# Kernel optimization log

Measured on AMD Instinct MI355X. Metric: run time of the kernel, lower is better.

The kernel has to match this reference:

```python
import jax, jax.numpy as jnp
import numpy as np
import math

B = 16384
INPUT = 2048
HIDDEN = 2048
PROJ = 1024


def setup_inputs() -> dict:
    key = jax.random.key(0)
    ks = jax.random.split(key, 20)
    stdv = 1.0 / math.sqrt(PROJ)
    u = lambda k, shape: jax.random.uniform(k, shape, jnp.float32, -stdv, stdv)
    return {
        "x_t": jax.random.normal(ks[0], (B, INPUT), jnp.float32),
        "h_t": jax.random.normal(ks[1], (B, PROJ), jnp.float32),
        "c_t": jax.random.normal(ks[2], (B, HIDDEN), jnp.float32),
        "weight_if_x": u(ks[3], (INPUT, 2 * HIDDEN)),
        "weight_if_h": u(ks[4], (PROJ, 2 * HIDDEN)),
        "weight_if_c": u(ks[5], (HIDDEN, 2 * HIDDEN)),
        "bias_i": u(ks[6], (HIDDEN,)),
        "bias_f": u(ks[7], (HIDDEN,)),
        "weight_c_x": u(ks[8], (INPUT, HIDDEN)),
        "weight_c_h": u(ks[9], (PROJ, HIDDEN)),
        "bias_c": u(ks[10], (HIDDEN,)),
        "weight_o_x": u(ks[11], (INPUT, PROJ)),
        "weight_o_h": u(ks[12], (PROJ, PROJ)),
        "weight_o_c": u(ks[13], (HIDDEN, PROJ)),
        "bias_o": u(ks[14], (PROJ,)),
        "weight_r_proj": u(ks[15], (HIDDEN, PROJ)),
        "weight_r_x": u(ks[16], (INPUT, PROJ)),
    }


def reference(x_t, h_t, c_t, weight_if_x, weight_if_h, weight_if_c, bias_i, bias_f,
              weight_c_x, weight_c_h, bias_c, weight_o_x, weight_o_h, weight_o_c,
              bias_o, weight_r_proj, weight_r_x):
    # input/forget gates with peephole on c_t: [B, 2*HIDDEN]
    if_gates = x_t @ weight_if_x + h_t @ weight_if_h + c_t @ weight_if_c
    ingate, forgetgate = jnp.split(if_gates, 2, axis=-1)
    ingate = jax.nn.sigmoid(ingate + bias_i)
    forgetgate = jax.nn.sigmoid(forgetgate + bias_f)
    cellgate = jnp.tanh(x_t @ weight_c_x + h_t @ weight_c_h + bias_c)
    c_new = forgetgate * c_t + ingate * cellgate
    # output gate peeps at new cell state
    outgate = jax.nn.sigmoid(x_t @ weight_o_x + h_t @ weight_o_h + c_new @ weight_o_c + bias_o)
    r_t = jnp.tanh(c_new)
    m_t = r_t @ weight_r_proj
    # input_size != proj_size -> project x for the residual connection
    h_new = outgate * (m_t + x_t @ weight_r_x)
    return (h_new, c_new)
```

## Files before the change

### kernel.cpp

```cpp
#include <hip/hip_runtime.h>
#include <hip/hip_bf16.h>
#include <math.h>

typedef unsigned short u16;
typedef __bf16 bf16x8_t __attribute__((ext_vector_type(8)));
typedef float  f32x4_t  __attribute__((ext_vector_type(4)));
typedef float  f32x8_t  __attribute__((ext_vector_type(8)));
typedef u16    u16x4_t  __attribute__((ext_vector_type(4)));
typedef u16    u16x8_t  __attribute__((ext_vector_type(8)));

__device__ __forceinline__ u16 f2b(float f) {
  unsigned u = __builtin_bit_cast(unsigned, f);
  u += 0x7fffu + ((u >> 16) & 1u);
  return (u16)(u >> 16);
}
__device__ __forceinline__ float b2f(u16 h) {
  unsigned u = ((unsigned)h) << 16;
  return __builtin_bit_cast(float, u);
}
__device__ __forceinline__ float sigm_(float x) { return 1.0f / (1.0f + __expf(-x)); }
__device__ __forceinline__ float tanh_(float x) { return 1.0f - 2.0f / (__expf(2.0f * x) + 1.0f); }

__device__ __forceinline__ void gload16(const void* g, void* l) {
  __builtin_amdgcn_global_load_lds(
      (__attribute__((address_space(1))) void*)(g),
      (__attribute__((address_space(3))) void*)(l), 16, 0, 0);
}


__global__ void cvt_act_kernel(const float* __restrict__ src, u16* __restrict__ dst,
                               int C, int KT, int c0) {
  int mb = blockIdx.x, ktl = blockIdx.y, t = threadIdx.x;
  int ktg = (c0 >> 5) + ktl;
  const float* s = src + (long)(mb * 256 + t) * C + ktl * 32;
  u16* d = dst + ((long)(mb * KT + ktg)) * 8192 + t * 8;
#pragma unroll
  for (int p = 0; p < 4; ++p) {
    f32x8_t v = *(const f32x8_t*)(s + p * 8);
    u16x8_t o;
#pragma unroll
    for (int r = 0; r < 8; ++r) o[r] = f2b(v[r]);
    *(u16x8_t*)(d + p * 2048) = o;
  }
}

__global__ void cvt_wt_kernel(const float* __restrict__ src, u16* __restrict__ dst,
                              int N, int KT, int n0, int k0) {
  int bx = blockIdx.x, by = blockIdx.y, t = threadIdx.x;
  int n = bx * 256 + t;
  int nb_g = (n0 >> 8) + bx;
  int ktg = (k0 >> 5) + by;
  float tmp[32];
#pragma unroll
  for (int kk = 0; kk < 32; ++kk)
    tmp[kk] = src[(long)(by * 32 + kk) * N + n];
  u16* d = dst + ((long)(nb_g * KT + ktg)) * 8192 + t * 8;
#pragma unroll
  for (int p = 0; p < 4; ++p) {
    u16x8_t o;
#pragma unroll
    for (int r = 0; r < 8; ++r) o[r] = f2b(tmp[p * 8 + r]);
    *(u16x8_t*)(d + p * 2048) = o;
  }
}

template <int MODE>
__global__ __launch_bounds__(512, 2) void gemm256_kernel(
    const u16* __restrict__ A, const u16* __restrict__ Bt, u16* __restrict__ Cout) {
  constexpr int KT   = (MODE == 0) ? 160 : 128;
  constexpr int NCOL = (MODE == 0) ? 8192 : 2048;
  constexpr int NBN  = NCOL / 256;
  constexpr int SLOT = 16384;

  __shared__ u16 lds[3 * SLOT];

  int bid = blockIdx.x;
  int cpx = gridDim.x >> 3;
  bid = (bid & 7) * cpx + (bid >> 3);

  int mb = bid / NBN, nb = bid % NBN;
  int m0 = mb * 256, n0 = nb * 256;

  int kt0, NT;
  if (MODE == 0) { kt0 = 0; NT = (nb < 16) ? 160 : ((nb < 28) ? 96 : 64); }
  else           { kt0 = (nb < 4) ? 0 : 64; NT = 64; }

  const int tid  = threadIdx.x;
  const int lane = tid & 63;
  const int wid  = tid >> 6;
  const int wr   = wid >> 2;
  const int wc   = wid & 3;

  const int segoff = wid * 512 + lane * 8;
  const u16* baseA = A  + ((long)(mb * KT + kt0)) * 8192 + segoff;
  const u16* baseB = Bt + ((long)(nb * KT + kt0)) * 8192 + segoff;

#define STAGE_A(t, s) do { \
    gload16(baseA + (long)(t) * 8192,        &lds[(s) * SLOT + segoff]); \
    gload16(baseA + (long)(t) * 8192 + 4096, &lds[(s) * SLOT + segoff + 4096]); } while (0)
#define STAGE_B(t, s) do { \
    gload16(baseB + (long)(t) * 8192,        &lds[(s) * SLOT + 8192 + segoff]); \
    gload16(baseB + (long)(t) * 8192 + 4096, &lds[(s) * SLOT + 8192 + segoff + 4096]); } while (0)

  const int aoff = (lane >> 4) * 2048 + (wr * 128 + (lane & 15)) * 8;
  const int boff = (lane >> 4) * 2048 + (wc * 64  + (lane & 15)) * 8;

  f32x4_t acc[8][4];
#pragma unroll
  for (int m = 0; m < 8; ++m)
#pragma unroll
    for (int n = 0; n < 4; ++n) acc[m][n] = (f32x4_t){0.f, 0.f, 0.f, 0.f};

  STAGE_A(0, 0); STAGE_B(0, 0);
  STAGE_A(1, 1); STAGE_B(1, 1);
  asm volatile("s_waitcnt vmcnt(4)" ::: "memory");
  __builtin_amdgcn_s_barrier();

  int slot = 0, s2 = 2;
  for (int t = 0; t < NT; ++t) {
    const u16* sA = &lds[slot * SLOT];
    const u16* sB = sA + 8192;
    const bool pre = (t + 2 < NT);

    if (pre) { STAGE_A(t + 2, s2); STAGE_B(t + 2, s2); }

    bf16x8_t bv[4], av[8];
#pragma unroll
    for (int n = 0; n < 4; ++n) bv[n] = *(const bf16x8_t*)&sB[boff + n * 128];
#pragma unroll
    for (int m = 0; m < 8; ++m) av[m] = *(const bf16x8_t*)&sA[aoff + m * 128];

    __builtin_amdgcn_s_setprio(1);
#pragma unroll
    for (int m = 0; m < 8; ++m)
#pragma unroll
      for (int n = 0; n < 4; ++n)
        acc[m][n] = __builtin_amdgcn_mfma_f32_16x16x32_bf16(bv[n], av[m], acc[m][n], 0, 0, 0);
    __builtin_amdgcn_s_setprio(0);

    if (pre) asm volatile("s_waitcnt vmcnt(4)" ::: "memory");
    else     asm volatile("s_waitcnt vmcnt(0)" ::: "memory");
    __builtin_amdgcn_s_barrier();

    slot = (slot == 2) ? 0 : slot + 1;
    s2   = (s2   == 2) ? 0 : s2   + 1;
  }
#undef STAGE_A
#undef STAGE_B

  const int rowm = lane & 15;
  const int col4 = (lane >> 4) * 4;
#pragma unroll
  for (int m = 0; m < 8; ++m) {
    long rg = (long)(m0 + wr * 128 + m * 16 + rowm) * NCOL;
#pragma unroll
    for (int n = 0; n < 4; ++n) {
      int cg = n0 + wc * 64 + n * 16 + col4;
      u16x4_t o;
#pragma unroll
      for (int r = 0; r < 4; ++r) o[r] = f2b(acc[m][n][r]);
      *(u16x4_t*)&Cout[rg + cg] = o;
    }
  }
}

__global__ void pass2_kernel(const u16* __restrict__ G1, const float* __restrict__ c_t,
                             const float* __restrict__ bias_i, const float* __restrict__ bias_f,
                             const float* __restrict__ bias_c,
                             float* __restrict__ c_new_out, u16* __restrict__ A2p) {
  int mb = blockIdx.x, jg = blockIdx.y, t = threadIdx.x;
  int b = mb * 256 + t;
  int j0 = jg * 32;
  const u16* row = G1 + (long)b * 8192 + j0;
  const float* cp_p = c_t + (long)b * 2048 + j0;
  float* co_p = c_new_out + (long)b * 2048 + j0;
  u16* dc = A2p + ((long)(mb * 128 + jg)) * 8192 + t * 8;
  u16* dr = dc + (long)64 * 8192;

#pragma unroll
  for (int q = 0; q < 4; ++q) {
    u16x8_t ip = *(const u16x8_t*)(row + q * 8);
    u16x8_t fp = *(const u16x8_t*)(row + 2048 + q * 8);
    u16x8_t gp = *(const u16x8_t*)(row + 4096 + q * 8);
    f32x8_t cp = *(const f32x8_t*)(cp_p + q * 8);
    f32x8_t bi = *(const f32x8_t*)(bias_i + j0 + q * 8);
    f32x8_t bf = *(const f32x8_t*)(bias_f + j0 + q * 8);
    f32x8_t bc = *(const f32x8_t*)(bias_c + j0 + q * 8);
    f32x8_t cn;
    u16x8_t cb, rb;
#pragma unroll
    for (int r = 0; r < 8; ++r) {
      float ig = sigm_(b2f(ip[r]) + bi[r]);
      float fg = sigm_(b2f(fp[r]) + bf[r]);
      float g  = tanh_(b2f(gp[r]) + bc[r]);
      float c  = fg * cp[r] + ig * g;
      cn[r] = c;
      cb[r] = f2b(c);
      rb[r] = f2b(tanh_(c));
    }
    *(f32x8_t*)(co_p + q * 8) = cn;
    *(u16x8_t*)(dc + q * 2048) = cb;
    *(u16x8_t*)(dr + q * 2048) = rb;
  }
}

__global__ void pass3_kernel(const u16* __restrict__ G1, const u16* __restrict__ G2,
                             const float* __restrict__ bias_o, float* __restrict__ h_out) {
  long i = (long)blockIdx.x * blockDim.x + threadIdx.x;
  long e = i * 8;
  int b = (int)(e >> 10);
  int j = (int)(e & 1023);
  const u16* row1 = G1 + (long)b * 8192;
  const u16* row2 = G2 + (long)b * 2048;
  u16x8_t ogp = *(const u16x8_t*)(row1 + 6144 + j);
  u16x8_t xrp = *(const u16x8_t*)(row1 + 7168 + j);
  u16x8_t ocg = *(const u16x8_t*)(row2 + j);
  u16x8_t mt  = *(const u16x8_t*)(row2 + 1024 + j);
  f32x8_t bo  = *(const f32x8_t*)(bias_o + j);
  f32x8_t h;
#pragma unroll
  for (int r = 0; r < 8; ++r) {
    float og = sigm_(b2f(ogp[r]) + b2f(ocg[r]) + bo[r]);
    h[r] = og * (b2f(mt[r]) + b2f(xrp[r]));
  }
  *(f32x8_t*)(h_out + (long)b * 1024 + j) = h;
}

extern "C" void kernel_launch(void* const* d_in, const int* in_sizes, int n_in,
                              void* d_out, int out_size, void* d_ws, size_t ws_size,
                              hipStream_t stream) {
  const float* x_t      = (const float*)d_in[0];
  const float* h_t      = (const float*)d_in[1];
  const float* c_t      = (const float*)d_in[2];
  const float* w_if_x   = (const float*)d_in[3];
  const float* w_if_h   = (const float*)d_in[4];
  const float* w_if_c   = (const float*)d_in[5];
  const float* bias_i   = (const float*)d_in[6];
  const float* bias_f   = (const float*)d_in[7];
  const float* w_c_x    = (const float*)d_in[8];
  const float* w_c_h    = (const float*)d_in[9];
  const float* bias_c   = (const float*)d_in[10];
  const float* w_o_x    = (const float*)d_in[11];
  const float* w_o_h    = (const float*)d_in[12];
  const float* w_o_c    = (const float*)d_in[13];
  const float* bias_o   = (const float*)d_in[14];
  const float* w_r_proj = (const float*)d_in[15];
  const float* w_r_x    = (const float*)d_in[16];

  char* ws = (char*)d_ws;
  u16* A1p  = (u16*)(ws);
  u16* W1tp = (u16*)(ws + 167772160L);
  u16* G1   = (u16*)(ws + 251658240L);
  u16* W2tp = (u16*)(ws + 520093696L);
  u16* A2p  = (u16*)(ws);
  u16* G2   = (u16*)(ws + 167772160L);

  float* h_out = (float*)d_out;
  float* c_out = h_out + 16384L * 1024L;

  cvt_act_kernel<<<dim3(64, 64), 256, 0, stream>>>(x_t, A1p, 2048, 160, 0);
  cvt_act_kernel<<<dim3(64, 32), 256, 0, stream>>>(h_t, A1p, 1024, 160, 2048);
  cvt_act_kernel<<<dim3(64, 64), 256, 0, stream>>>(c_t, A1p, 2048, 160, 3072);

  cvt_wt_kernel<<<dim3(16, 64), 256, 0, stream>>>(w_if_x,   W1tp, 4096, 160, 0,    0);
  cvt_wt_kernel<<<dim3(16, 32), 256, 0, stream>>>(w_if_h,   W1tp, 4096, 160, 0,    2048);
  cvt_wt_kernel<<<dim3(16, 64), 256, 0, stream>>>(w_if_c,   W1tp, 4096, 160, 0,    3072);
  cvt_wt_kernel<<<dim3(8,  64), 256, 0, stream>>>(w_c_x,    W1tp, 2048, 160, 4096, 0);
  cvt_wt_kernel<<<dim3(8,  32), 256, 0, stream>>>(w_c_h,    W1tp, 2048, 160, 4096, 2048);
  cvt_wt_kernel<<<dim3(4,  64), 256, 0, stream>>>(w_o_x,    W1tp, 1024, 160, 6144, 0);
  cvt_wt_kernel<<<dim3(4,  32), 256, 0, stream>>>(w_o_h,    W1tp, 1024, 160, 6144, 2048);
  cvt_wt_kernel<<<dim3(4,  64), 256, 0, stream>>>(w_r_x,    W1tp, 1024, 160, 7168, 0);
  cvt_wt_kernel<<<dim3(4,  64), 256, 0, stream>>>(w_o_c,    W2tp, 1024, 128, 0,    0);
  cvt_wt_kernel<<<dim3(4,  64), 256, 0, stream>>>(w_r_proj, W2tp, 1024, 128, 1024, 2048);

  gemm256_kernel<0><<<2048, 512, 0, stream>>>(A1p, W1tp, G1);

  pass2_kernel<<<dim3(64, 64), 256, 0, stream>>>(G1, c_t, bias_i, bias_f, bias_c, c_out, A2p);

  gemm256_kernel<1><<<512, 512, 0, stream>>>(A2p, W2tp, G2);

  pass3_kernel<<<8192, 256, 0, stream>>>(G1, G2, bias_o, h_out);
}
```

Measured before the change: 1.501 ms.

## Restructure GEMM mainloop into double-buffered two-tile phases with interleaved loads

Replaces the three-slot single-k-tile LDS ring in the bf16 GEMM with a double buffer that holds two k-tiles per iteration, halving the loop trip counts. Each iteration is split into four phases of 16 MFMAs over half the A rows. Each phase issues part of the next iteration's global-to-LDS loads, with barriers, lgkmcnt waits and sched_barriers between phases. The aim is to spread memory traffic across the compute and keep the MFMA pipe fed. The cost is many more barriers per iteration and a larger LDS footprint (128KB), which may limit occupancy.

Result: no change. 1.510 ms (+0.6%).

```diff
diff --git a/kernel.cpp b/kernel.cpp
--- a/kernel.cpp
+++ b/kernel.cpp
@@ -67,12 +67,11 @@
 template <int MODE>
 __global__ __launch_bounds__(512, 2) void gemm256_kernel(
     const u16* __restrict__ A, const u16* __restrict__ Bt, u16* __restrict__ Cout) {
-  constexpr int KT   = (MODE == 0) ? 160 : 128;
+  constexpr int KTF  = (MODE == 0) ? 160 : 128;
   constexpr int NCOL = (MODE == 0) ? 8192 : 2048;
   constexpr int NBN  = NCOL / 256;
-  constexpr int SLOT = 16384;
-
-  __shared__ u16 lds[3 * SLOT];
+
+  __shared__ u16 lds[2 * 4 * 8192];
 
   int bid = blockIdx.x;
   int cpx = gridDim.x >> 3;
@@ -82,8 +81,8 @@
   int m0 = mb * 256, n0 = nb * 256;
 
   int kt0, NT;
-  if (MODE == 0) { kt0 = 0; NT = (nb < 16) ? 160 : ((nb < 28) ? 96 : 64); }
-  else           { kt0 = (nb < 4) ? 0 : 64; NT = 64; }
+  if (MODE == 0) { kt0 = 0; NT = (nb < 16) ? 80 : ((nb < 28) ? 48 : 32); }
+  else           { kt0 = (nb < 4) ? 0 : 64; NT = 32; }
 
   const int tid  = threadIdx.x;
   const int lane = tid & 63;
@@ -91,16 +90,16 @@
   const int wr   = wid >> 2;
   const int wc   = wid & 3;
 
-  const int segoff = wid * 512 + lane * 8;
-  const u16* baseA = A  + ((long)(mb * KT + kt0)) * 8192 + segoff;
-  const u16* baseB = Bt + ((long)(nb * KT + kt0)) * 8192 + segoff;
-
-#define STAGE_A(t, s) do { \
-    gload16(baseA + (long)(t) * 8192,        &lds[(s) * SLOT + segoff]); \
-    gload16(baseA + (long)(t) * 8192 + 4096, &lds[(s) * SLOT + segoff + 4096]); } while (0)
-#define STAGE_B(t, s) do { \
-    gload16(baseB + (long)(t) * 8192,        &lds[(s) * SLOT + 8192 + segoff]); \
-    gload16(baseB + (long)(t) * 8192 + 4096, &lds[(s) * SLOT + 8192 + segoff + 4096]); } while (0)
+  const u16* pA = A  + ((long)(mb * KTF + kt0)) * 8192 + tid * 8;
+  const u16* pB = Bt + ((long)(nb * KTF + kt0)) * 8192 + tid * 8;
+  const int dstg = tid * 8;
+
+#define STG_A(buf, it, j, h) \
+    gload16(pA + ((long)(2 * (it) + (j))) * 8192 + (h) * 4096, \
+            &lds[(buf) * 32768 + (j) * 8192 + (h) * 4096 + dstg])
+#define STG_B(buf, it, j, h) \
+    gload16(pB + ((long)(2 * (it) + (j))) * 8192 + (h) * 4096, \
+            &lds[(buf) * 32768 + (2 + (j)) * 8192 + (h) * 4096 + dstg])
 
   const int aoff = (lane >> 4) * 2048 + (wr * 128 + (lane & 15)) * 8;
   const int boff = (lane >> 4) * 2048 + (wc * 64  + (lane & 15)) * 8;
@@ -111,42 +110,90 @@
 #pragma unroll
     for (int n = 0; n < 4; ++n) acc[m][n] = (f32x4_t){0.f, 0.f, 0.f, 0.f};
 
-  STAGE_A(0, 0); STAGE_B(0, 0);
-  STAGE_A(1, 1); STAGE_B(1, 1);
+  STG_A(0, 0, 0, 0); STG_A(0, 0, 0, 1);
+  STG_B(0, 0, 0, 0); STG_B(0, 0, 0, 1);
+  STG_A(0, 0, 1, 0); STG_A(0, 0, 1, 1);
+  STG_B(0, 0, 1, 0); STG_B(0, 0, 1, 1);
   asm volatile("s_waitcnt vmcnt(4)" ::: "memory");
   __builtin_amdgcn_s_barrier();
 
-  int slot = 0, s2 = 2;
   for (int t = 0; t < NT; ++t) {
-    const u16* sA = &lds[slot * SLOT];
-    const u16* sB = sA + 8192;
-    const bool pre = (t + 2 < NT);
-
-    if (pre) { STAGE_A(t + 2, s2); STAGE_B(t + 2, s2); }
-
-    bf16x8_t bv[4], av[8];
-#pragma unroll
-    for (int n = 0; n < 4; ++n) bv[n] = *(const bf16x8_t*)&sB[boff + n * 128];
-#pragma unroll
-    for (int m = 0; m < 8; ++m) av[m] = *(const bf16x8_t*)&sA[aoff + m * 128];
-
+    const int buf = t & 1, nxt = buf ^ 1;
+    const u16* sb = &lds[buf * 32768];
+    const bool pre = (t + 1 < NT);
+
+    bf16x8_t bv[4], av[4];
+
+#pragma unroll
+    for (int n = 0; n < 4; ++n) bv[n] = *(const bf16x8_t*)&sb[2 * 8192 + boff + n * 128];
+#pragma unroll
+    for (int m = 0; m < 4; ++m) av[m] = *(const bf16x8_t*)&sb[aoff + m * 128];
+    if (pre) { STG_A(nxt, t + 1, 0, 0); STG_A(nxt, t + 1, 0, 1); }
+    __builtin_amdgcn_s_barrier();
+    asm volatile("s_waitcnt lgkmcnt(0)" ::: "memory");
+    __builtin_amdgcn_sched_barrier(0);
     __builtin_amdgcn_s_setprio(1);
 #pragma unroll
-    for (int m = 0; m < 8; ++m)
+    for (int m = 0; m < 4; ++m)
 #pragma unroll
       for (int n = 0; n < 4; ++n)
         acc[m][n] = __builtin_amdgcn_mfma_f32_16x16x32_bf16(bv[n], av[m], acc[m][n], 0, 0, 0);
     __builtin_amdgcn_s_setprio(0);
-
+    __builtin_amdgcn_s_barrier();
+
+#pragma unroll
+    for (int m = 0; m < 4; ++m) av[m] = *(const bf16x8_t*)&sb[aoff + 512 + m * 128];
+    if (pre) { STG_B(nxt, t + 1, 0, 0); STG_B(nxt, t + 1, 0, 1); }
+    __builtin_amdgcn_s_barrier();
+    asm volatile("s_waitcnt lgkmcnt(0)" ::: "memory");
+    __builtin_amdgcn_sched_barrier(0);
+    __builtin_amdgcn_s_setprio(1);
+#pragma unroll
+    for (int m = 0; m < 4; ++m)
+#pragma unroll
+      for (int n = 0; n < 4; ++n)
+        acc[m + 4][n] = __builtin_amdgcn_mfma_f32_16x16x32_bf16(bv[n], av[m], acc[m + 4][n], 0, 0, 0);
+    __builtin_amdgcn_s_setprio(0);
     if (pre) asm volatile("s_waitcnt vmcnt(4)" ::: "memory");
     else     asm volatile("s_waitcnt vmcnt(0)" ::: "memory");
     __builtin_amdgcn_s_barrier();
 
-    slot = (slot == 2) ? 0 : slot + 1;
-    s2   = (s2   == 2) ? 0 : s2   + 1;
-  }
-#undef STAGE_A
-#undef STAGE_B
+#pragma unroll
+    for (int n = 0; n < 4; ++n) bv[n] = *(const bf16x8_t*)&sb[3 * 8192 + boff + n * 128];
+#pragma unroll
+    for (int m = 0; m < 4; ++m) av[m] = *(const bf16x8_t*)&sb[8192 + aoff + m * 128];
+    if (pre) { STG_A(nxt, t + 1, 1, 0); STG_A(nxt, t + 1, 1, 1); }
+    __builtin_amdgcn_s_barrier();
+    asm volatile("s_waitcnt lgkmcnt(0)" ::: "memory");
+    __builtin_amdgcn_sched_barrier(0);
+    __builtin_amdgcn_s_setprio(1);
+#pragma unroll
+    for (int m = 0; m < 4; ++m)
+#pragma unroll
+      for (int n = 0; n < 4; ++n)
+        acc[m][n] = __builtin_amdgcn_mfma_f32_16x16x32_bf16(bv[n], av[m], acc[m][n], 0, 0, 0);
+    __builtin_amdgcn_s_setprio(0);
+    __builtin_amdgcn_s_barrier();
+
+#pragma unroll
+    for (int m = 0; m < 4; ++m) av[m] = *(const bf16x8_t*)&sb[8192 + aoff + 512 + m * 128];
+    if (pre) { STG_B(nxt, t + 1, 1, 0); STG_B(nxt, t + 1, 1, 1); }
+    __builtin_amdgcn_s_barrier();
+    asm volatile("s_waitcnt lgkmcnt(0)" ::: "memory");
+    __builtin_amdgcn_sched_barrier(0);
+    __builtin_amdgcn_s_setprio(1);
+#pragma unroll
+    for (int m = 0; m < 4; ++m)
+#pragma unroll
+      for (int n = 0; n < 4; ++n)
+        acc[m + 4][n] = __builtin_amdgcn_mfma_f32_16x16x32_bf16(bv[n], av[m], acc[m + 4][n], 0, 0, 0);
+    __builtin_amdgcn_s_setprio(0);
+    if (pre) asm volatile("s_waitcnt vmcnt(4)" ::: "memory");
+    else     asm volatile("s_waitcnt vmcnt(0)" ::: "memory");
+    __builtin_amdgcn_s_barrier();
+  }
+#undef STG_A
+#undef STG_B
 
   const int rowm = lane & 15;
   const int col4 = (lane >> 4) * 4;
```

## Switch GEMM to 32x32x16 MFMA with 64-deep K steps and double buffering

Applied to the files above, without the earlier changes.

Rewrites the bf16 GEMM main loop to use 32x32x16 MFMA instructions instead of 16x16x32. Each iteration now stages two K-tiles (64 deep) into a 2-buffer LDS ring instead of one tile into a 3-slot ring, which halves the trip count. LDS fragment reads and global prefetches are interleaved with MFMA groups. The larger MFMA shape means fewer LDS reads per FLOP and fewer barriers, at the cost of a shallower prefetch pipeline, a full vmcnt(0) wait every iteration, and a larger 128KB LDS footprint that may reduce occupancy.

Result: slower. 1.634 ms (+8.9%).

```diff
diff --git a/kernel.cpp b/kernel.cpp
--- a/kernel.cpp
+++ b/kernel.cpp
@@ -6,6 +6,7 @@
 typedef __bf16 bf16x8_t __attribute__((ext_vector_type(8)));
 typedef float  f32x4_t  __attribute__((ext_vector_type(4)));
 typedef float  f32x8_t  __attribute__((ext_vector_type(8)));
+typedef float  f32x16_t __attribute__((ext_vector_type(16)));
 typedef u16    u16x4_t  __attribute__((ext_vector_type(4)));
 typedef u16    u16x8_t  __attribute__((ext_vector_type(8)));
 
@@ -67,12 +68,11 @@
 template <int MODE>
 __global__ __launch_bounds__(512, 2) void gemm256_kernel(
     const u16* __restrict__ A, const u16* __restrict__ Bt, u16* __restrict__ Cout) {
-  constexpr int KT   = (MODE == 0) ? 160 : 128;
+  constexpr int KTF  = (MODE == 0) ? 160 : 128;
   constexpr int NCOL = (MODE == 0) ? 8192 : 2048;
   constexpr int NBN  = NCOL / 256;
-  constexpr int SLOT = 16384;
-
-  __shared__ u16 lds[3 * SLOT];
+
+  __shared__ u16 lds[2 * 32768];
 
   int bid = blockIdx.x;
   int cpx = gridDim.x >> 3;
@@ -82,84 +82,101 @@
   int m0 = mb * 256, n0 = nb * 256;
 
   int kt0, NT;
-  if (MODE == 0) { kt0 = 0; NT = (nb < 16) ? 160 : ((nb < 28) ? 96 : 64); }
-  else           { kt0 = (nb < 4) ? 0 : 64; NT = 64; }
+  if (MODE == 0) { kt0 = 0; NT = (nb < 16) ? 80 : ((nb < 28) ? 48 : 32); }
+  else           { kt0 = (nb < 4) ? 0 : 64; NT = 32; }
 
   const int tid  = threadIdx.x;
   const int lane = tid & 63;
   const int wid  = tid >> 6;
   const int wr   = wid >> 2;
   const int wc   = wid & 3;
-
-  const int segoff = wid * 512 + lane * 8;
-  const u16* baseA = A  + ((long)(mb * KT + kt0)) * 8192 + segoff;
-  const u16* baseB = Bt + ((long)(nb * KT + kt0)) * 8192 + segoff;
-
-#define STAGE_A(t, s) do { \
-    gload16(baseA + (long)(t) * 8192,        &lds[(s) * SLOT + segoff]); \
-    gload16(baseA + (long)(t) * 8192 + 4096, &lds[(s) * SLOT + segoff + 4096]); } while (0)
-#define STAGE_B(t, s) do { \
-    gload16(baseB + (long)(t) * 8192,        &lds[(s) * SLOT + 8192 + segoff]); \
-    gload16(baseB + (long)(t) * 8192 + 4096, &lds[(s) * SLOT + 8192 + segoff + 4096]); } while (0)
-
-  const int aoff = (lane >> 4) * 2048 + (wr * 128 + (lane & 15)) * 8;
-  const int boff = (lane >> 4) * 2048 + (wc * 64  + (lane & 15)) * 8;
-
-  f32x4_t acc[8][4];
-#pragma unroll
-  for (int m = 0; m < 8; ++m)
-#pragma unroll
-    for (int n = 0; n < 4; ++n) acc[m][n] = (f32x4_t){0.f, 0.f, 0.f, 0.f};
-
-  STAGE_A(0, 0); STAGE_B(0, 0);
-  STAGE_A(1, 1); STAGE_B(1, 1);
-  asm volatile("s_waitcnt vmcnt(4)" ::: "memory");
+  const int l31  = lane & 31;
+  const int hl   = lane >> 5;
+
+  const int dstg = tid * 8;
+  const u16* pA = A  + ((long)(mb * KTF + kt0)) * 8192 + dstg;
+  const u16* pB = Bt + ((long)(nb * KTF + kt0)) * 8192 + dstg;
+
+#define STG(bufb, tt, g) do { \
+    gload16(pA + ((long)(2 * (tt))) * 8192 + (g) * 4096, \
+            &lds[(bufb) * 32768 + (g) * 4096 + dstg]); \
+    gload16(pB + ((long)(2 * (tt))) * 8192 + (g) * 4096, \
+            &lds[(bufb) * 32768 + 16384 + (g) * 4096 + dstg]); } while (0)
+
+  const int xbase = (wr * 128 + l31) * 8;
+  const int wbase = (wc * 64  + l31) * 8;
+
+  struct Frag { bf16x8_t x0, x1, x2, x3, w0, w1; };
+  Frag fA, fB;
+
+#define RD(F, sbp, ks) do { \
+    const u16* _t = (sbp) + (2 * (ks) + hl) * 2048; \
+    F.x0 = *(const bf16x8_t*)(_t + xbase); \
+    F.x1 = *(const bf16x8_t*)(_t + xbase + 256); \
+    F.x2 = *(const bf16x8_t*)(_t + xbase + 512); \
+    F.x3 = *(const bf16x8_t*)(_t + xbase + 768); \
+    F.w0 = *(const bf16x8_t*)(_t + 16384 + wbase); \
+    F.w1 = *(const bf16x8_t*)(_t + 16384 + wbase + 256); } while (0)
+
+#define MM(F) do { \
+    acc[0][0] = __builtin_amdgcn_mfma_f32_32x32x16_bf16(F.w0, F.x0, acc[0][0], 0, 0, 0); \
+    acc[0][1] = __builtin_amdgcn_mfma_f32_32x32x16_bf16(F.w1, F.x0, acc[0][1], 0, 0, 0); \
+    acc[1][0] = __builtin_amdgcn_mfma_f32_32x32x16_bf16(F.w0, F.x1, acc[1][0], 0, 0, 0); \
+    acc[1][1] = __builtin_amdgcn_mfma_f32_32x32x16_bf16(F.w1, F.x1, acc[1][1], 0, 0, 0); \
+    acc[2][0] = __builtin_amdgcn_mfma_f32_32x32x16_bf16(F.w0, F.x2, acc[2][0], 0, 0, 0); \
+    acc[2][1] = __builtin_amdgcn_mfma_f32_32x32x16_bf16(F.w1, F.x2, acc[2][1], 0, 0, 0); \
+    acc[3][0] = __builtin_amdgcn_mfma_f32_32x32x16_bf16(F.w0, F.x3, acc[3][0], 0, 0, 0); \
+    acc[3][1] = __builtin_amdgcn_mfma_f32_32x32x16_bf16(F.w1, F.x3, acc[3][1], 0, 0, 0); } while (0)
+
+  f32x16_t acc[4][2];
+#pragma unroll
+  for (int m = 0; m < 4; ++m)
+#pragma unroll
+    for (int n = 0; n < 2; ++n)
+#pragma unroll
+      for (int r = 0; r < 16; ++r) acc[m][n][r] = 0.f;
+
+  STG(0, 0, 0); STG(0, 0, 1); STG(0, 0, 2); STG(0, 0, 3);
+  asm volatile("s_waitcnt vmcnt(0)" ::: "memory");
   __builtin_amdgcn_s_barrier();
 
-  int slot = 0, s2 = 2;
   for (int t = 0; t < NT; ++t) {
-    const u16* sA = &lds[slot * SLOT];
-    const u16* sB = sA + 8192;
-    const bool pre = (t + 2 < NT);
-
-    if (pre) { STAGE_A(t + 2, s2); STAGE_B(t + 2, s2); }
-
-    bf16x8_t bv[4], av[8];
-#pragma unroll
-    for (int n = 0; n < 4; ++n) bv[n] = *(const bf16x8_t*)&sB[boff + n * 128];
-#pragma unroll
-    for (int m = 0; m < 8; ++m) av[m] = *(const bf16x8_t*)&sA[aoff + m * 128];
-
-    __builtin_amdgcn_s_setprio(1);
-#pragma unroll
-    for (int m = 0; m < 8; ++m)
-#pragma unroll
-      for (int n = 0; n < 4; ++n)
-        acc[m][n] = __builtin_amdgcn_mfma_f32_16x16x32_bf16(bv[n], av[m], acc[m][n], 0, 0, 0);
-    __builtin_amdgcn_s_setprio(0);
-
-    if (pre) asm volatile("s_waitcnt vmcnt(4)" ::: "memory");
-    else     asm volatile("s_waitcnt vmcnt(0)" ::: "memory");
+    const int buf = t & 1;
+    const u16* sb = &lds[buf * 32768];
+    const bool pre = (t + 1 < NT);
+
+    RD(fA, sb, 0);
+    RD(fB, sb, 1);
+    if (pre) { STG(buf ^ 1, t + 1, 0); STG(buf ^ 1, t + 1, 1); }
+    __builtin_amdgcn_s_setprio(1); MM(fA); __builtin_amdgcn_s_setprio(0);
+    RD(fA, sb, 2);
+    if (pre) { STG(buf ^ 1, t + 1, 2); STG(buf ^ 1, t + 1, 3); }
+    __builtin_amdgcn_s_setprio(1); MM(fB); __builtin_amdgcn_s_setprio(0);
+    RD(fB, sb, 3);
+    __builtin_amdgcn_s_setprio(1); MM(fA); __builtin_amdgcn_s_setprio(0);
+    __builtin_amdgcn_s_setprio(1); MM(fB); __builtin_amdgcn_s_setprio(0);
+
+    asm volatile("s_waitcnt vmcnt(0)" ::: "memory");
     __builtin_amdgcn_s_barrier();
-
-    slot = (slot == 2) ? 0 : slot + 1;
-    s2   = (s2   == 2) ? 0 : s2   + 1;
-  }
-#undef STAGE_A
-#undef STAGE_B
-
-  const int rowm = lane & 15;
-  const int col4 = (lane >> 4) * 4;
-#pragma unroll
-  for (int m = 0; m < 8; ++m) {
-    long rg = (long)(m0 + wr * 128 + m * 16 + rowm) * NCOL;
-#pragma unroll
-    for (int n = 0; n < 4; ++n) {
-      int cg = n0 + wc * 64 + n * 16 + col4;
-      u16x4_t o;
-#pragma unroll
-      for (int r = 0; r < 4; ++r) o[r] = f2b(acc[m][n][r]);
-      *(u16x4_t*)&Cout[rg + cg] = o;
+  }
+#undef STG
+#undef RD
+#undef MM
+
+  const long rowg = (long)(m0 + wr * 128 + l31);
+  const int  colg = n0 + wc * 64 + 4 * hl;
+#pragma unroll
+  for (int mm = 0; mm < 4; ++mm) {
+    long rb = (rowg + mm * 32) * (long)NCOL;
+#pragma unroll
+    for (int nn = 0; nn < 2; ++nn) {
+#pragma unroll
+      for (int g = 0; g < 4; ++g) {
+        u16x4_t o;
+#pragma unroll
+        for (int r = 0; r < 4; ++r) o[r] = f2b(acc[mm][nn][g * 4 + r]);
+        *(u16x4_t*)&Cout[rb + colg + nn * 32 + g * 8] = o;
+      }
     }
   }
 }
```

## Shrink GEMM tile to 128x256 and switch to 32x32x16 MFMA

Applied to the files above, without the earlier changes.

The GEMM tile's M dimension is halved to 128 rows, so both GEMMs launch twice as many workgroups. The 16x16x32 MFMA is replaced with 32x32x16 bf16 MFMA using 2x2 accumulators per wave, and launch bounds now target 4 blocks per CU with a smaller LDS slot. The activation and pass2 packing layouts change to 128-row blocks to match. The aim is better occupancy and fewer LDS reads per MFMA, at the cost of lower A/B reuse per tile and more redundant weight traffic.

After: 1.950 ms. 30.0% more time.

```diff
diff --git a/kernel.cpp b/kernel.cpp
--- a/kernel.cpp
+++ b/kernel.cpp
@@ -6,6 +6,7 @@
 typedef __bf16 bf16x8_t __attribute__((ext_vector_type(8)));
 typedef float  f32x4_t  __attribute__((ext_vector_type(4)));
 typedef float  f32x8_t  __attribute__((ext_vector_type(8)));
+typedef float  f32x16_t __attribute__((ext_vector_type(16)));
 typedef u16    u16x4_t  __attribute__((ext_vector_type(4)));
 typedef u16    u16x8_t  __attribute__((ext_vector_type(8)));
 
@@ -30,17 +31,18 @@
 
 __global__ void cvt_act_kernel(const float* __restrict__ src, u16* __restrict__ dst,
                                int C, int KT, int c0) {
-  int mb = blockIdx.x, ktl = blockIdx.y, t = threadIdx.x;
-  int ktg = (c0 >> 5) + ktl;
-  const float* s = src + (long)(mb * 256 + t) * C + ktl * 32;
-  u16* d = dst + ((long)(mb * KT + ktg)) * 8192 + t * 8;
+  int mbg = blockIdx.x, t = threadIdx.x;
+  int row = t & 127;
+  int ktl = blockIdx.y * 2 + (t >> 7);
+  const float* s = src + (long)(mbg * 128 + row) * C + ktl * 32;
+  u16* d = dst + ((long)(mbg * KT + (c0 >> 5) + ktl)) * 4096 + row * 8;
 #pragma unroll
   for (int p = 0; p < 4; ++p) {
     f32x8_t v = *(const f32x8_t*)(s + p * 8);
     u16x8_t o;
 #pragma unroll
     for (int r = 0; r < 8; ++r) o[r] = f2b(v[r]);
-    *(u16x8_t*)(d + p * 2048) = o;
+    *(u16x8_t*)(d + p * 1024) = o;
   }
 }
 
@@ -65,12 +67,12 @@
 }
 
 template <int MODE>
-__global__ __launch_bounds__(512, 2) void gemm256_kernel(
+__global__ __launch_bounds__(512, 4) void gemm128_kernel(
     const u16* __restrict__ A, const u16* __restrict__ Bt, u16* __restrict__ Cout) {
-  constexpr int KT   = (MODE == 0) ? 160 : 128;
+  constexpr int KTF  = (MODE == 0) ? 160 : 128;
   constexpr int NCOL = (MODE == 0) ? 8192 : 2048;
   constexpr int NBN  = NCOL / 256;
-  constexpr int SLOT = 16384;
+  constexpr int SLOT = 12288;
 
   __shared__ u16 lds[3 * SLOT];
 
@@ -79,7 +81,7 @@
   bid = (bid & 7) * cpx + (bid >> 3);
 
   int mb = bid / NBN, nb = bid % NBN;
-  int m0 = mb * 256, n0 = nb * 256;
+  int m0 = mb * 128, n0 = nb * 256;
 
   int kt0, NT;
   if (MODE == 0) { kt0 = 0; NT = (nb < 16) ? 160 : ((nb < 28) ? 96 : 64); }
@@ -90,76 +92,78 @@
   const int wid  = tid >> 6;
   const int wr   = wid >> 2;
   const int wc   = wid & 3;
-
-  const int segoff = wid * 512 + lane * 8;
-  const u16* baseA = A  + ((long)(mb * KT + kt0)) * 8192 + segoff;
-  const u16* baseB = Bt + ((long)(nb * KT + kt0)) * 8192 + segoff;
-
-#define STAGE_A(t, s) do { \
-    gload16(baseA + (long)(t) * 8192,        &lds[(s) * SLOT + segoff]); \
-    gload16(baseA + (long)(t) * 8192 + 4096, &lds[(s) * SLOT + segoff + 4096]); } while (0)
-#define STAGE_B(t, s) do { \
-    gload16(baseB + (long)(t) * 8192,        &lds[(s) * SLOT + 8192 + segoff]); \
-    gload16(baseB + (long)(t) * 8192 + 4096, &lds[(s) * SLOT + 8192 + segoff + 4096]); } while (0)
-
-  const int aoff = (lane >> 4) * 2048 + (wr * 128 + (lane & 15)) * 8;
-  const int boff = (lane >> 4) * 2048 + (wc * 64  + (lane & 15)) * 8;
-
-  f32x4_t acc[8][4];
-#pragma unroll
-  for (int m = 0; m < 8; ++m)
-#pragma unroll
-    for (int n = 0; n < 4; ++n) acc[m][n] = (f32x4_t){0.f, 0.f, 0.f, 0.f};
-
-  STAGE_A(0, 0); STAGE_B(0, 0);
-  STAGE_A(1, 1); STAGE_B(1, 1);
-  asm volatile("s_waitcnt vmcnt(4)" ::: "memory");
+  const int l31  = lane & 31;
+  const int hl   = lane >> 5;
+
+  const int dstg = tid * 8;
+  const u16* pA = A  + ((long)(mb * KTF + kt0)) * 4096 + dstg;
+  const u16* pB = Bt + ((long)(nb * KTF + kt0)) * 8192 + dstg;
+
+#define STG(s, tt) do { \
+    gload16(pA + (long)(tt) * 4096,        &lds[(s) * SLOT + dstg]); \
+    gload16(pB + (long)(tt) * 8192,        &lds[(s) * SLOT + 4096 + dstg]); \
+    gload16(pB + (long)(tt) * 8192 + 4096, &lds[(s) * SLOT + 8192 + dstg]); } while (0)
+
+  const int xb = (wr * 64 + l31) * 8;
+  const int wb = (wc * 64 + l31) * 8;
+
+  f32x16_t acc[2][2];
+#pragma unroll
+  for (int m = 0; m < 2; ++m)
+#pragma unroll
+    for (int n = 0; n < 2; ++n)
+#pragma unroll
+      for (int r = 0; r < 16; ++r) acc[m][n][r] = 0.f;
+
+  STG(0, 0); STG(1, 1);
+  asm volatile("s_waitcnt vmcnt(3)" ::: "memory");
   __builtin_amdgcn_s_barrier();
 
   int slot = 0, s2 = 2;
   for (int t = 0; t < NT; ++t) {
-    const u16* sA = &lds[slot * SLOT];
-    const u16* sB = sA + 8192;
+    const u16* sb = &lds[slot * SLOT];
     const bool pre = (t + 2 < NT);
-
-    if (pre) { STAGE_A(t + 2, s2); STAGE_B(t + 2, s2); }
-
-    bf16x8_t bv[4], av[8];
-#pragma unroll
-    for (int n = 0; n < 4; ++n) bv[n] = *(const bf16x8_t*)&sB[boff + n * 128];
-#pragma unroll
-    for (int m = 0; m < 8; ++m) av[m] = *(const bf16x8_t*)&sA[aoff + m * 128];
-
-    __builtin_amdgcn_s_setprio(1);
-#pragma unroll
-    for (int m = 0; m < 8; ++m)
-#pragma unroll
-      for (int n = 0; n < 4; ++n)
-        acc[m][n] = __builtin_amdgcn_mfma_f32_16x16x32_bf16(bv[n], av[m], acc[m][n], 0, 0, 0);
-    __builtin_amdgcn_s_setprio(0);
-
-    if (pre) asm volatile("s_waitcnt vmcnt(4)" ::: "memory");
+    if (pre) STG(s2, t + 2);
+
+#pragma unroll
+    for (int ks = 0; ks < 2; ++ks) {
+      const u16* ta = sb + (2 * ks + hl) * 1024;
+      const u16* tb = sb + 4096 + (2 * ks + hl) * 2048;
+      bf16x8_t x0 = *(const bf16x8_t*)(ta + xb);
+      bf16x8_t x1 = *(const bf16x8_t*)(ta + xb + 256);
+      bf16x8_t w0 = *(const bf16x8_t*)(tb + wb);
+      bf16x8_t w1 = *(const bf16x8_t*)(tb + wb + 256);
+      __builtin_amdgcn_s_setprio(1);
+      acc[0][0] = __builtin_amdgcn_mfma_f32_32x32x16_bf16(w0, x0, acc[0][0], 0, 0, 0);
+      acc[0][1] = __builtin_amdgcn_mfma_f32_32x32x16_bf16(w1, x0, acc[0][1], 0, 0, 0);
+      acc[1][0] = __builtin_amdgcn_mfma_f32_32x32x16_bf16(w0, x1, acc[1][0], 0, 0, 0);
+      acc[1][1] = __builtin_amdgcn_mfma_f32_32x32x16_bf16(w1, x1, acc[1][1], 0, 0, 0);
+      __builtin_amdgcn_s_setprio(0);
+    }
+
+    if (pre) asm volatile("s_waitcnt vmcnt(3)" ::: "memory");
     else     asm volatile("s_waitcnt vmcnt(0)" ::: "memory");
     __builtin_amdgcn_s_barrier();
 
     slot = (slot == 2) ? 0 : slot + 1;
     s2   = (s2   == 2) ? 0 : s2   + 1;
   }
-#undef STAGE_A
-#undef STAGE_B
-
-  const int rowm = lane & 15;
-  const int col4 = (lane >> 4) * 4;
-#pragma unroll
-  for (int m = 0; m < 8; ++m) {
-    long rg = (long)(m0 + wr * 128 + m * 16 + rowm) * NCOL;
-#pragma unroll
-    for (int n = 0; n < 4; ++n) {
-      int cg = n0 + wc * 64 + n * 16 + col4;
-      u16x4_t o;
-#pragma unroll
-      for (int r = 0; r < 4; ++r) o[r] = f2b(acc[m][n][r]);
-      *(u16x4_t*)&Cout[rg + cg] = o;
+#undef STG
+
+  const long rowg = (long)(m0 + wr * 64 + l31);
+  const int  colg = n0 + wc * 64 + 4 * hl;
+#pragma unroll
+  for (int mm = 0; mm < 2; ++mm) {
+    long rb = (rowg + mm * 32) * (long)NCOL;
+#pragma unroll
+    for (int nn = 0; nn < 2; ++nn) {
+#pragma unroll
+      for (int g = 0; g < 4; ++g) {
+        u16x4_t o;
+#pragma unroll
+        for (int r = 0; r < 4; ++r) o[r] = f2b(acc[mm][nn][g * 4 + r]);
+        *(u16x4_t*)&Cout[rb + colg + nn * 32 + g * 8] = o;
+      }
     }
   }
 }
@@ -168,20 +172,22 @@
                              const float* __restrict__ bias_i, const float* __restrict__ bias_f,
                              const float* __restrict__ bias_c,
                              float* __restrict__ c_new_out, u16* __restrict__ A2p) {
-  int mb = blockIdx.x, jg = blockIdx.y, t = threadIdx.x;
-  int b = mb * 256 + t;
+  int mb = blockIdx.x, t = threadIdx.x;
+  int row = t & 127;
+  int jg = blockIdx.y * 2 + (t >> 7);
+  int b = mb * 128 + row;
   int j0 = jg * 32;
-  const u16* row = G1 + (long)b * 8192 + j0;
+  const u16* grow = G1 + (long)b * 8192 + j0;
   const float* cp_p = c_t + (long)b * 2048 + j0;
   float* co_p = c_new_out + (long)b * 2048 + j0;
-  u16* dc = A2p + ((long)(mb * 128 + jg)) * 8192 + t * 8;
-  u16* dr = dc + (long)64 * 8192;
+  u16* dc = A2p + ((long)(mb * 128 + jg)) * 4096 + row * 8;
+  u16* dr = dc + (long)64 * 4096;
 
 #pragma unroll
   for (int q = 0; q < 4; ++q) {
-    u16x8_t ip = *(const u16x8_t*)(row + q * 8);
-    u16x8_t fp = *(const u16x8_t*)(row + 2048 + q * 8);
-    u16x8_t gp = *(const u16x8_t*)(row + 4096 + q * 8);
+    u16x8_t ip = *(const u16x8_t*)(grow + q * 8);
+    u16x8_t fp = *(const u16x8_t*)(grow + 2048 + q * 8);
+    u16x8_t gp = *(const u16x8_t*)(grow + 4096 + q * 8);
     f32x8_t cp = *(const f32x8_t*)(cp_p + q * 8);
     f32x8_t bi = *(const f32x8_t*)(bias_i + j0 + q * 8);
     f32x8_t bf = *(const f32x8_t*)(bias_f + j0 + q * 8);
@@ -199,8 +205,8 @@
       rb[r] = f2b(tanh_(c));
     }
     *(f32x8_t*)(co_p + q * 8) = cn;
-    *(u16x8_t*)(dc + q * 2048) = cb;
-    *(u16x8_t*)(dr + q * 2048) = rb;
+    *(u16x8_t*)(dc + q * 1024) = cb;
+    *(u16x8_t*)(dr + q * 1024) = rb;
   }
 }
 
@@ -258,9 +264,9 @@
   float* h_out = (float*)d_out;
   float* c_out = h_out + 16384L * 1024L;
 
-  cvt_act_kernel<<<dim3(64, 64), 256, 0, stream>>>(x_t, A1p, 2048, 160, 0);
-  cvt_act_kernel<<<dim3(64, 32), 256, 0, stream>>>(h_t, A1p, 1024, 160, 2048);
-  cvt_act_kernel<<<dim3(64, 64), 256, 0, stream>>>(c_t, A1p, 2048, 160, 3072);
+  cvt_act_kernel<<<dim3(128, 32), 256, 0, stream>>>(x_t, A1p, 2048, 160, 0);
+  cvt_act_kernel<<<dim3(128, 16), 256, 0, stream>>>(h_t, A1p, 1024, 160, 2048);
+  cvt_act_kernel<<<dim3(128, 32), 256, 0, stream>>>(c_t, A1p, 2048, 160, 3072);
 
   cvt_wt_kernel<<<dim3(16, 64), 256, 0, stream>>>(w_if_x,   W1tp, 4096, 160, 0,    0);
   cvt_wt_kernel<<<dim3(16, 32), 256, 0, stream>>>(w_if_h,   W1tp, 4096, 160, 0,    2048);
@@ -273,11 +279,11 @@
   cvt_wt_kernel<<<dim3(4,  64), 256, 0, stream>>>(w_o_c,    W2tp, 1024, 128, 0,    0);
   cvt_wt_kernel<<<dim3(4,  64), 256, 0, stream>>>(w_r_proj, W2tp, 1024, 128, 1024, 2048);
 
-  gemm256_kernel<0><<<2048, 512, 0, stream>>>(A1p, W1tp, G1);
-
-  pass2_kernel<<<dim3(64, 64), 256, 0, stream>>>(G1, c_t, bias_i, bias_f, bias_c, c_out, A2p);
-
-  gemm256_kernel<1><<<512, 512, 0, stream>>>(A2p, W2tp, G2);
+  gemm128_kernel<0><<<4096, 512, 0, stream>>>(A1p, W1tp, G1);
+
+  pass2_kernel<<<dim3(128, 32), 256, 0, stream>>>(G1, c_t, bias_i, bias_f, bias_c, c_out, A2p);
+
+  gemm128_kernel<1><<<1024, 512, 0, stream>>>(A2p, W2tp, G2);
 
   pass3_kernel<<<8192, 256, 0, stream>>>(G1, G2, bias_o, h_out);
 }
```
